# Performance work log

Measured on AMD Instinct MI355X. Metric: run time of the kernel, lower is better.

## Reference

```python
import jax, jax.numpy as jnp
import numpy as np
import math

N = 8192
NFEAT = 63
NHID = 1024
NLAYERS = 7
LAMBDA = 1.5
ALPHA = 0.7
NEG = -1e12


def setup_inputs() -> dict:
    key = jax.random.key(0)
    ks = jax.random.split(key, 12)
    x = jax.random.normal(ks[0], (N, NFEAT), dtype=jnp.float32)
    # dist acts as a (normalized) propagation matrix; scale by 1/N for numerical stability
    dist = jax.random.uniform(ks[1], (N, N), dtype=jnp.float32) / N
    adj = jax.random.randint(ks[2], (N, N), 0, 2, dtype=jnp.int32)
    # parameters
    fc_W = jax.random.normal(ks[3], (NFEAT, NHID), dtype=jnp.float32) * 0.1
    fc_b = jnp.zeros((NHID,), dtype=jnp.float32)
    stdv = 1.0 / math.sqrt(NHID)
    conv_W = jax.random.uniform(ks[4], (NLAYERS, NHID, NHID), dtype=jnp.float32,
                                minval=-stdv, maxval=stdv)
    gat_W = jax.random.normal(ks[5], (NHID, NHID), dtype=jnp.float32) * (1.414 / math.sqrt(NHID))
    gat_a = jax.random.normal(ks[6], (2 * NHID, 1), dtype=jnp.float32) * 0.05
    cls1_W = jax.random.normal(ks[7], (NHID, 64), dtype=jnp.float32) * (1.0 / math.sqrt(NHID))
    cls1_b = jnp.zeros((64,), dtype=jnp.float32)
    cls3_W = jax.random.normal(ks[8], (64, 1), dtype=jnp.float32) * 0.125
    cls3_b = jnp.zeros((1,), dtype=jnp.float32)
    return {"x": x, "dist": dist, "adj": adj, "fc_W": fc_W, "fc_b": fc_b,
            "conv_W": conv_W, "gat_W": gat_W, "gat_a": gat_a,
            "cls1_W": cls1_W, "cls1_b": cls1_b, "cls3_W": cls3_W, "cls3_b": cls3_b}


def _theta(l):
    return min(1.0, math.log(LAMBDA / l + 1.0))


def reference(x, dist, adj, fc_W, fc_b, conv_W, gat_W, gat_a, cls1_W, cls1_b, cls3_W, cls3_b):
    # eval mode: all dropouts are identity
    h = jax.nn.relu(x @ fc_W + fc_b)          # [N, H]
    h0 = h
    # GCNII-style propagation layers
    for i in range(NLAYERS):
        theta = _theta(i + 1)
        hi = dist @ h                          # [N, H] sparse-style propagation
        support = (1.0 - ALPHA) * hi + ALPHA * h0
        out = theta * (support @ conv_W[i]) + (1.0 - theta) * support + h
        h = jax.nn.relu(out)
    # GAT layer (l = 9). Faithful math, but computed without the N*N*2F tensor:
    # e_ij = leakyrelu(h_i' @ a1 + h_j' @ a2) with h' = h @ W
    hp = h @ gat_W                             # [N, H]
    a1 = gat_a[:NHID, 0]                       # [H]
    a2 = gat_a[NHID:, 0]                       # [H]
    e = jax.nn.leaky_relu(hp @ a1[:, None] + (hp @ a2[:, None]).T, negative_slope=0.2)  # [N, N]
    e = jnp.where(adj > 0, e, NEG)
    attention = jax.nn.softmax(e, axis=1)      # [N, N]
    theta = _theta(9)
    hi = attention @ h                         # note: attends over layer input h, not hp
    support = (1.0 - ALPHA) * hi + ALPHA * h0
    out = theta * (support @ gat_W) + (1.0 - theta) * support + h
    h = jax.nn.elu(out)
    h = jax.nn.relu(h @ cls1_W + cls1_b)
    out = jax.nn.sigmoid(h @ cls3_W + cls3_b)  # [N, 1]
    return out.squeeze(-1)                     # [N]
```

## Files before the change

### kernel.cpp

```cpp
#include <hip/hip_runtime.h>
#include <math.h>

#define NN 8192
#define NH 1024

typedef __bf16 bf16x8 __attribute__((ext_vector_type(8)));
typedef float floatx4 __attribute__((ext_vector_type(4)));
typedef unsigned short us8 __attribute__((ext_vector_type(8)));
typedef unsigned short us;

__device__ __forceinline__ unsigned short f2bf(float f) {
  unsigned int u = __float_as_uint(f);
  u += 0x7fffu + ((u >> 16) & 1u);
  return (unsigned short)(u >> 16);
}

__device__ __forceinline__ void async16(const void* g, void* l) {
  __builtin_amdgcn_global_load_lds(
      (__attribute__((address_space(1))) void*)(g),
      (__attribute__((address_space(3))) void*)(l), 16, 0, 0);
}

template<int EPI>
__global__ __launch_bounds__(256)
void gemm_db(const us* __restrict__ A, const us* __restrict__ Bt, int K,
             const float* __restrict__ aux, float* __restrict__ iof,
             us* __restrict__ outb, us* __restrict__ hTb, float theta)
{
  __shared__ __align__(16) us lsm[EPI == 1 ? 17408 : 16384];
  const int id = blockIdx.x;
  const int xcd = id & 7, slot = id >> 3;
  const int xt = slot & 7;
  const int yt = xcd + 8 * (slot >> 3);

  const int tid  = threadIdx.x;
  const int lane = tid & 63;
  const int wave = tid >> 6;
  const long tileM = (long)yt * 128;
  const long tileN = (long)xt * 128;
  const int wm = (wave & 1) * 64;
  const int wn = (wave >> 1) * 64;

  const us* gA0 = A + (tileM + (tid >> 2)) * (long)K + (tid & 3) * 8;
  const us* gA1 = gA0 + 64L * K;
  const us* gB0 = Bt + (tileN + (tid >> 2)) * (long)K + (tid & 3) * 8;
  const us* gB1 = gB0 + 64L * K;
  us* lA = lsm;
  us* lB = lsm + 8192;
  const int lo = tid * 8;

  const int fr = lane & 15;
  const int q8 = (lane >> 4) * 8;

  floatx4 zero4 = {0.f, 0.f, 0.f, 0.f};
  floatx4 acc[4][4];
#pragma unroll
  for (int i = 0; i < 4; ++i)
#pragma unroll
    for (int j = 0; j < 4; ++j) acc[i][j] = zero4;

  async16(gA0, lA + lo);
  async16(gA1, lA + lo + 2048);
  async16(gB0, lB + lo);
  async16(gB1, lB + lo + 2048);

  const int nkt = K >> 5;
  for (int kt = 0; kt < nkt; ++kt) {
    const int b = (kt & 1) << 12;
    __syncthreads();
    if (kt + 1 < nkt) {
      const int k0 = (kt + 1) << 5;
      const int b2 = b ^ 4096;
      async16(gA0 + k0, lA + b2 + lo);
      async16(gA1 + k0, lA + b2 + lo + 2048);
      async16(gB0 + k0, lB + b2 + lo);
      async16(gB1 + k0, lB + b2 + lo + 2048);
    }
    bf16x8 af[4], bfr[4];
#pragma unroll
    for (int i = 0; i < 4; ++i)
      af[i] = *(const bf16x8*)&lA[b + (wm + 16 * i + fr) * 32 + q8];
#pragma unroll
    for (int j = 0; j < 4; ++j)
      bfr[j] = *(const bf16x8*)&lB[b + (wn + 16 * j + fr) * 32 + q8];
#pragma unroll
    for (int i = 0; i < 4; ++i)
#pragma unroll
      for (int j = 0; j < 4; ++j)
        acc[i][j] = __builtin_amdgcn_mfma_f32_16x16x32_bf16(af[i], bfr[j], acc[i][j], 0, 0, 0);
  }

  if (EPI == 1) __syncthreads();
  us* ldsT = lsm;
  const int crow = (lane >> 4) * 4;
#pragma unroll
  for (int i = 0; i < 4; ++i) {
#pragma unroll
    for (int j = 0; j < 4; ++j) {
#pragma unroll
      for (int r = 0; r < 4; ++r) {
        int lr = wm + 16 * i + crow + r;
        int lc = wn + 16 * j + fr;
        long idx = (tileM + lr) * NH + tileN + lc;
        float v = acc[i][j][r];
        if (EPI == 0) {
          float s = 0.3f * v + 0.7f * aux[idx];
          iof[idx] = s;
          outb[idx] = f2bf(s);
        } else {
          float o = theta * v + (1.f - theta) * aux[idx] + iof[idx];
          o = (EPI == 1) ? fmaxf(o, 0.f) : (o > 0.f ? o : __expf(o) - 1.f);
          iof[idx] = o;
          if (EPI == 1) ldsT[lc * 136 + lr] = f2bf(o);
          if (EPI == 2) outb[idx] = f2bf(o);
        }
      }
    }
  }
  if (EPI == 1) {
    __syncthreads();
    int c = tid >> 1, half = tid & 1;
#pragma unroll
    for (int it = 0; it < 8; ++it) {
      int r = half * 64 + it * 8;
      us8 v = *(const us8*)&ldsT[c * 136 + r];
      *(us8*)&hTb[(tileN + c) * 8192L + tileM + r] = v;
    }
  }
}

__global__ __launch_bounds__(256)
void cls_gemm(const us* __restrict__ hb, const us* __restrict__ W1t,
              const float* __restrict__ b1, const float* __restrict__ W3,
              const float* __restrict__ b3, float* __restrict__ out)
{
  __shared__ __align__(16) us lA[4096];
  __shared__ __align__(16) us lB[2048];
  const int tid = threadIdx.x, lane = tid & 63, wave = tid >> 6;
  const long tileM = (long)blockIdx.x * 128;
  const us* gA0 = hb + (tileM + (tid >> 2)) * 1024L + (tid & 3) * 8;
  const us* gA1 = gA0 + 64 * 1024L;
  const us* gB0 = W1t + (tid >> 2) * 1024L + (tid & 3) * 8;
  const int fr = lane & 15, q8 = (lane >> 4) * 8;
  const int wm = wave * 32;

  floatx4 zero4 = {0.f, 0.f, 0.f, 0.f};
  floatx4 acc[2][4];
#pragma unroll
  for (int i = 0; i < 2; ++i)
#pragma unroll
    for (int j = 0; j < 4; ++j) acc[i][j] = zero4;

  for (int kt = 0; kt < 32; ++kt) {
    const int k0 = kt << 5;
    async16(gA0 + k0, lA + tid * 8);
    async16(gA1 + k0, lA + 2048 + tid * 8);
    async16(gB0 + k0, lB + tid * 8);
    __syncthreads();
    bf16x8 af[2], bfr[4];
#pragma unroll
    for (int i = 0; i < 2; ++i)
      af[i] = *(const bf16x8*)&lA[(wm + 16 * i + fr) * 32 + q8];
#pragma unroll
    for (int j = 0; j < 4; ++j)
      bfr[j] = *(const bf16x8*)&lB[(16 * j + fr) * 32 + q8];
#pragma unroll
    for (int i = 0; i < 2; ++i)
#pragma unroll
      for (int j = 0; j < 4; ++j)
        acc[i][j] = __builtin_amdgcn_mfma_f32_16x16x32_bf16(af[i], bfr[j], acc[i][j], 0, 0, 0);
    __syncthreads();
  }

  float b1v[4], w3v[4];
#pragma unroll
  for (int j = 0; j < 4; ++j) { b1v[j] = b1[16 * j + fr]; w3v[j] = W3[16 * j + fr]; }
  const float b3v = b3[0];
  const int crow = (lane >> 4) * 4;
#pragma unroll
  for (int i = 0; i < 2; ++i)
#pragma unroll
    for (int r = 0; r < 4; ++r) {
      float v = 0.f;
#pragma unroll
      for (int j = 0; j < 4; ++j)
        v += fmaxf(acc[i][j][r] + b1v[j], 0.f) * w3v[j];
      v += __shfl_xor(v, 1);
      v += __shfl_xor(v, 2);
      v += __shfl_xor(v, 4);
      v += __shfl_xor(v, 8);
      if (fr == 0)
        out[tileM + wm + 16 * i + crow + r] = 1.f / (1.f + __expf(-(v + b3v)));
    }
}

__global__ __launch_bounds__(256)
void transpose_f32_bf16(const float* __restrict__ src, us* __restrict__ dst,
                        int R, int C) {
  __shared__ float t[32][33];
  int tid = threadIdx.x;
  int tx = tid & 31, ty = tid >> 5;
  long r0 = (long)blockIdx.y * 32, c0 = (long)blockIdx.x * 32;
#pragma unroll
  for (int i = 0; i < 32; i += 8)
    t[ty + i][tx] = src[(r0 + ty + i) * C + c0 + tx];
  __syncthreads();
#pragma unroll
  for (int i = 0; i < 32; i += 8)
    dst[(c0 + ty + i) * R + r0 + tx] = f2bf(t[tx][ty + i]);
}

__global__ __launch_bounds__(256)
void f32_to_bf16_vec(const float* __restrict__ s, us* __restrict__ d) {
  long i = (blockIdx.x * 256L + threadIdx.x) * 4;
  float4 v = *(const float4*)(s + i);
  *(ushort4*)(d + i) = make_ushort4(f2bf(v.x), f2bf(v.y), f2bf(v.z), f2bf(v.w));
}

__global__ __launch_bounds__(256)
void fc_kernel(const float* __restrict__ x, const float* __restrict__ W,
               const float* __restrict__ b, float* __restrict__ h0f,
               float* __restrict__ hf) {
  __shared__ float xs[64];
  int row = blockIdx.x, tid = threadIdx.x;
  if (tid < 63) xs[tid] = x[row * 63 + tid];
  __syncthreads();
#pragma unroll
  for (int q = 0; q < 4; ++q) {
    int c = tid + q * 256;
    float s = b[c];
    for (int k = 0; k < 63; ++k) s += xs[k] * W[k * NH + c];
    s = fmaxf(s, 0.f);
    long idx = (long)row * NH + c;
    h0f[idx] = s;
    hf[idx] = s;
  }
}

__global__ __launch_bounds__(256)
void wv_kernel(const float* __restrict__ W, const float* __restrict__ a,
               float* __restrict__ va1, float* __restrict__ va2) {
  int k = blockIdx.x, tid = threadIdx.x;
  float s1 = 0.f, s2 = 0.f;
  for (int n = tid; n < NH; n += 256) {
    float w = W[(long)k * NH + n];
    s1 += w * a[n];
    s2 += w * a[NH + n];
  }
#pragma unroll
  for (int o = 32; o; o >>= 1) { s1 += __shfl_down(s1, o); s2 += __shfl_down(s2, o); }
  __shared__ float r1[4], r2[4];
  int wave = tid >> 6;
  if ((tid & 63) == 0) { r1[wave] = s1; r2[wave] = s2; }
  __syncthreads();
  if (tid == 0) {
    va1[k] = r1[0] + r1[1] + r1[2] + r1[3];
    va2[k] = r2[0] + r2[1] + r2[2] + r2[3];
  }
}

__global__ __launch_bounds__(256)
void fg_kernel(const float* __restrict__ h, const float* __restrict__ va1,
               const float* __restrict__ va2, float* __restrict__ fv,
               float* __restrict__ gv) {
  int row = blockIdx.x, tid = threadIdx.x;
  float s1 = 0.f, s2 = 0.f;
  for (int k = tid; k < NH; k += 256) {
    float v = h[(long)row * NH + k];
    s1 += v * va1[k];
    s2 += v * va2[k];
  }
#pragma unroll
  for (int o = 32; o; o >>= 1) { s1 += __shfl_down(s1, o); s2 += __shfl_down(s2, o); }
  __shared__ float r1[4], r2[4];
  int wave = tid >> 6;
  if ((tid & 63) == 0) { r1[wave] = s1; r2[wave] = s2; }
  __syncthreads();
  if (tid == 0) {
    fv[row] = r1[0] + r1[1] + r1[2] + r1[3];
    gv[row] = r2[0] + r2[1] + r2[2] + r2[3];
  }
}

__global__ __launch_bounds__(256)
void attn_ml(const int* __restrict__ adj, const float* __restrict__ f,
             const float* __restrict__ g, float* __restrict__ Mr,
             float* __restrict__ Lr) {
  const int row = blockIdx.x, tid = threadIdx.x;
  const float fi = f[row];
  const int4* arow = (const int4*)(adj + (long)row * NN);
  float m = -3.0e38f, s = 0.f;
  for (int c = tid; c < NN / 4; c += 256) {
    int4 a = arow[c];
    float4 gg = *(const float4*)(g + c * 4);
#pragma unroll
    for (int t = 0; t < 4; ++t) {
      int av = (t == 0) ? a.x : (t == 1) ? a.y : (t == 2) ? a.z : a.w;
      float gvv = (t == 0) ? gg.x : (t == 1) ? gg.y : (t == 2) ? gg.z : gg.w;
      if (av > 0) {
        float e = fi + gvv;
        e = e > 0.f ? e : 0.2f * e;
        if (e > m) { s = s * __expf(m - e) + 1.f; m = e; }
        else s += __expf(e - m);
      }
    }
  }
#pragma unroll
  for (int o = 32; o; o >>= 1) {
    float m2 = __shfl_down(m, o), s2 = __shfl_down(s, o);
    float mn = fmaxf(m, m2);
    s = s * __expf(m - mn) + s2 * __expf(m2 - mn);
    m = mn;
  }
  __shared__ float ms[4], ss[4];
  int wave = tid >> 6;
  if ((tid & 63) == 0) { ms[wave] = m; ss[wave] = s; }
  __syncthreads();
  if (tid == 0) {
    float mm = ms[0], sv = ss[0];
    for (int w = 1; w < 4; ++w) {
      float mn = fmaxf(mm, ms[w]);
      sv = sv * __expf(mm - mn) + ss[w] * __expf(ms[w] - mn);
      mm = mn;
    }
    Mr[row] = mm;
    Lr[row] = sv;
  }
}

__global__ __launch_bounds__(256)
void attn_p(const int* __restrict__ adj, const float* __restrict__ f,
            const float* __restrict__ g, const float* __restrict__ Mr,
            const float* __restrict__ Lr, us* __restrict__ P) {
  long gid = blockIdx.x * 256L + threadIdx.x;
  int row = (int)(gid >> 11);
  int jc = (int)(gid & 2047) * 4;
  float fi = f[row], m = Mr[row], l = Lr[row];
  bool uni = !(l > 0.f);
  float inv = uni ? 0.f : 1.f / l;
  int4 a = *(const int4*)(adj + ((long)row << 13) + jc);
  float4 gg = *(const float4*)(g + jc);
  float p[4];
#pragma unroll
  for (int t = 0; t < 4; ++t) {
    int av = (t == 0) ? a.x : (t == 1) ? a.y : (t == 2) ? a.z : a.w;
    float gvv = (t == 0) ? gg.x : (t == 1) ? gg.y : (t == 2) ? gg.z : gg.w;
    float e = fi + gvv;
    e = e > 0.f ? e : 0.2f * e;
    float pv = (av > 0) ? __expf(e - m) * inv : 0.f;
    if (uni) pv = 1.f / (float)NN;
    p[t] = pv;
  }
  *(ushort4*)(P + ((long)row << 13) + jc) =
      make_ushort4(f2bf(p[0]), f2bf(p[1]), f2bf(p[2]), f2bf(p[3]));
}

extern "C" void kernel_launch(void* const* d_in, const int* in_sizes, int n_in,
                              void* d_out, int out_size, void* d_ws, size_t ws_size,
                              hipStream_t stream) {
  const float* x      = (const float*)d_in[0];
  const float* dist   = (const float*)d_in[1];
  const int*   adj    = (const int*)d_in[2];
  const float* fc_W   = (const float*)d_in[3];
  const float* fc_b   = (const float*)d_in[4];
  const float* conv_W = (const float*)d_in[5];
  const float* gat_W  = (const float*)d_in[6];
  const float* gat_a  = (const float*)d_in[7];
  const float* cls1_W = (const float*)d_in[8];
  const float* cls1_b = (const float*)d_in[9];
  const float* cls3_W = (const float*)d_in[10];
  const float* cls3_b = (const float*)d_in[11];
  float* out = (float*)d_out;

  char* p = (char*)d_ws;
  auto alloc = [&](size_t bytes) {
    char* r = p;
    p += (bytes + 255) & ~(size_t)255;
    return r;
  };
  us* distb   = (us*)alloc((size_t)NN * NN * 2);
  float* h0f  = (float*)alloc((size_t)NN * NH * 4);
  float* hf   = (float*)alloc((size_t)NN * NH * 4);
  float* supf = (float*)alloc((size_t)NN * NH * 4);
  us* supb    = (us*)alloc((size_t)NN * NH * 2);
  us* hb      = (us*)alloc((size_t)NN * NH * 2);
  us* hTb     = (us*)alloc((size_t)NN * NH * 2);
  us* convWT  = (us*)alloc((size_t)7 * NH * NH * 2);
  us* gatWT   = (us*)alloc((size_t)NH * NH * 2);
  us* W1t     = (us*)alloc((size_t)64 * NH * 2);
  float* va1 = (float*)alloc(NH * 4);
  float* va2 = (float*)alloc(NH * 4);
  float* fv  = (float*)alloc(NN * 4);
  float* gv  = (float*)alloc(NN * 4);
  float* Mr  = (float*)alloc(NN * 4);
  float* Lr  = (float*)alloc(NN * 4);

  float th[7];
  for (int l = 0; l < 7; ++l) {
    float t = logf(1.5f / (float)(l + 1) + 1.f);
    th[l] = t < 1.f ? t : 1.f;
  }
  float th9 = logf(1.5f / 9.f + 1.f);

  f32_to_bf16_vec<<<(NN * (long)NN) / (4 * 256), 256, 0, stream>>>(dist, distb);
  for (int i = 0; i < 7; ++i)
    transpose_f32_bf16<<<dim3(32, 32), 256, 0, stream>>>(
        conv_W + (size_t)i * NH * NH, convWT + (size_t)i * NH * NH, NH, NH);
  transpose_f32_bf16<<<dim3(32, 32), 256, 0, stream>>>(gat_W, gatWT, NH, NH);
  transpose_f32_bf16<<<dim3(2, 32), 256, 0, stream>>>(cls1_W, W1t, NH, 64);

  fc_kernel<<<NN, 256, 0, stream>>>(x, fc_W, fc_b, h0f, hf);
  transpose_f32_bf16<<<dim3(NH / 32, NN / 32), 256, 0, stream>>>(hf, hTb, NN, NH);

  for (int l = 0; l < 7; ++l) {
    gemm_db<0><<<512, 256, 0, stream>>>(distb, hTb, NN, h0f, supf, supb, nullptr, 0.f);
    gemm_db<1><<<512, 256, 0, stream>>>(supb, convWT + (size_t)l * NH * NH, NH,
                                        supf, hf, nullptr, hTb, th[l]);
  }

  wv_kernel<<<NH, 256, 0, stream>>>(gat_W, gat_a, va1, va2);
  fg_kernel<<<NN, 256, 0, stream>>>(hf, va1, va2, fv, gv);
  attn_ml<<<NN, 256, 0, stream>>>(adj, fv, gv, Mr, Lr);
  attn_p<<<(NN * (long)NN) / (4 * 256), 256, 0, stream>>>(adj, fv, gv, Mr, Lr, distb);

  gemm_db<0><<<512, 256, 0, stream>>>(distb, hTb, NN, h0f, supf, supb, nullptr, 0.f);
  gemm_db<2><<<512, 256, 0, stream>>>(supb, gatWT, NH, supf, hf, hb, nullptr, th9);

  cls_gemm<<<64, 256, 0, stream>>>(hb, W1t, cls1_b, cls3_W, cls3_b, out);
}
```

Measured before the change: 2.510 ms.

## Add 256x128-tile GEMM with 4-stage async pipeline for propagation matmuls

```diff
diff --git a/kernel.cpp b/kernel.cpp
--- a/kernel.cpp
+++ b/kernel.cpp
@@ -19,6 +19,102 @@
   __builtin_amdgcn_global_load_lds(
       (__attribute__((address_space(1))) void*)(g),
       (__attribute__((address_space(3))) void*)(l), 16, 0, 0);
+}
+
+__global__ __launch_bounds__(256)
+void gemm_big(const us* __restrict__ A, const us* __restrict__ Bt,
+              const float* __restrict__ aux, float* __restrict__ supf,
+              us* __restrict__ supb)
+{
+  __shared__ __align__(16) us lsm[49152];
+  us* lB = lsm;
+  us* lA = lsm + 16384;
+
+  const int id = blockIdx.x;
+  const int yt = id & 31;
+  const int xt = id >> 5;
+
+  const int tid  = threadIdx.x;
+  const int lane = tid & 63;
+  const int wave = tid >> 6;
+  const long tileM = (long)yt * 256;
+  const long tileN = (long)xt * 128;
+  const int wm = (wave & 1) * 128;
+  const int wn = (wave >> 1) * 64;
+
+  const us* gAp = A + (tileM + (tid >> 2)) * 8192L + (tid & 3) * 8;
+  const us* gBp = Bt + (tileN + (tid >> 2)) * 8192L + (tid & 3) * 8;
+  const int lo = tid * 8;
+
+  const int fr = lane & 15;
+  const int q8 = (lane >> 4) * 8;
+
+  floatx4 zero4 = {0.f, 0.f, 0.f, 0.f};
+  floatx4 acc[8][4];
+#pragma unroll
+  for (int i = 0; i < 8; ++i)
+#pragma unroll
+    for (int j = 0; j < 4; ++j) acc[i][j] = zero4;
+
+#define STAGE_BIG(s, kf)                                                  \
+  {                                                                       \
+    const long ko = (long)(kf) << 5;                                      \
+    async16(gAp + ko, lA + (s)*8192 + lo);                                \
+    async16(gAp + 64 * 8192L + ko, lA + (s)*8192 + 2048 + lo);            \
+    async16(gAp + 128 * 8192L + ko, lA + (s)*8192 + 4096 + lo);           \
+    async16(gAp + 192 * 8192L + ko, lA + (s)*8192 + 6144 + lo);           \
+    async16(gBp + ko, lB + (s)*4096 + lo);                                \
+    async16(gBp + 64 * 8192L + ko, lB + (s)*4096 + 2048 + lo);            \
+  }
+
+#define COMP_BIG(s)                                                       \
+  {                                                                       \
+    bf16x8 af[8], bfr[4];                                                 \
+    _Pragma("unroll") for (int i = 0; i < 8; ++i)                         \
+        af[i] = *(const bf16x8*)&lA[(s)*8192 + (wm + 16 * i + fr) * 32 + q8]; \
+    _Pragma("unroll") for (int j = 0; j < 4; ++j)                         \
+        bfr[j] = *(const bf16x8*)&lB[(s)*4096 + (wn + 16 * j + fr) * 32 + q8]; \
+    _Pragma("unroll") for (int i = 0; i < 8; ++i)                         \
+        _Pragma("unroll") for (int j = 0; j < 4; ++j)                     \
+            acc[i][j] = __builtin_amdgcn_mfma_f32_16x16x32_bf16(          \
+                af[i], bfr[j], acc[i][j], 0, 0, 0);                       \
+  }
+
+#define WAITB asm volatile("s_waitcnt vmcnt(12)\n\ts_barrier" ::: "memory")
+
+  STAGE_BIG(0, 0)
+  STAGE_BIG(1, 1)
+  STAGE_BIG(2, 2)
+
+  for (int kt = 0; kt < 256; kt += 4) {
+    int k3 = kt + 3; if (k3 > 255) k3 = 255;
+    int k4 = kt + 4; if (k4 > 255) k4 = 255;
+    int k5 = kt + 5; if (k5 > 255) k5 = 255;
+    int k6 = kt + 6; if (k6 > 255) k6 = 255;
+    WAITB; STAGE_BIG(3, k3) COMP_BIG(0)
+    WAITB; STAGE_BIG(0, k4) COMP_BIG(1)
+    WAITB; STAGE_BIG(1, k5) COMP_BIG(2)
+    WAITB; STAGE_BIG(2, k6) COMP_BIG(3)
+  }
+  asm volatile("s_waitcnt vmcnt(0)" ::: "memory");
+
+  const int crow = (lane >> 4) * 4;
+#pragma unroll
+  for (int i = 0; i < 8; ++i)
+#pragma unroll
+    for (int j = 0; j < 4; ++j)
+#pragma unroll
+      for (int r = 0; r < 4; ++r) {
+        long row = tileM + wm + 16 * i + crow + r;
+        long col = tileN + wn + 16 * j + fr;
+        long idx = row * NH + col;
+        float s = 0.3f * acc[i][j][r] + 0.7f * aux[idx];
+        supf[idx] = s;
+        supb[idx] = f2bf(s);
+      }
+#undef STAGE_BIG
+#undef COMP_BIG
+#undef WAITB
 }
 
 template<int EPI>
@@ -90,7 +186,7 @@
         acc[i][j] = __builtin_amdgcn_mfma_f32_16x16x32_bf16(af[i], bfr[j], acc[i][j], 0, 0, 0);
   }
 
-  if (EPI == 1) __syncthreads();
+  __syncthreads();
   us* ldsT = lsm;
   const int crow = (lane >> 4) * 4;
 #pragma unroll
@@ -102,18 +198,11 @@
         int lr = wm + 16 * i + crow + r;
         int lc = wn + 16 * j + fr;
         long idx = (tileM + lr) * NH + tileN + lc;
-        float v = acc[i][j][r];
-        if (EPI == 0) {
-          float s = 0.3f * v + 0.7f * aux[idx];
-          iof[idx] = s;
-          outb[idx] = f2bf(s);
-        } else {
-          float o = theta * v + (1.f - theta) * aux[idx] + iof[idx];
-          o = (EPI == 1) ? fmaxf(o, 0.f) : (o > 0.f ? o : __expf(o) - 1.f);
-          iof[idx] = o;
-          if (EPI == 1) ldsT[lc * 136 + lr] = f2bf(o);
-          if (EPI == 2) outb[idx] = f2bf(o);
-        }
+        float o = theta * acc[i][j][r] + (1.f - theta) * aux[idx] + iof[idx];
+        o = (EPI == 1) ? fmaxf(o, 0.f) : (o > 0.f ? o : __expf(o) - 1.f);
+        iof[idx] = o;
+        if (EPI == 1) ldsT[lc * 136 + lr] = f2bf(o);
+        if (EPI == 2) outb[idx] = f2bf(o);
       }
     }
   }
@@ -413,7 +502,7 @@
   transpose_f32_bf16<<<dim3(NH / 32, NN / 32), 256, 0, stream>>>(hf, hTb, NN, NH);
 
   for (int l = 0; l < 7; ++l) {
-    gemm_db<0><<<512, 256, 0, stream>>>(distb, hTb, NN, h0f, supf, supb, nullptr, 0.f);
+    gemm_big<<<256, 256, 0, stream>>>(distb, hTb, h0f, supf, supb);
     gemm_db<1><<<512, 256, 0, stream>>>(supb, convWT + (size_t)l * NH * NH, NH,
                                         supf, hf, nullptr, hTb, th[l]);
   }
@@ -423,7 +512,7 @@
   attn_ml<<<NN, 256, 0, stream>>>(adj, fv, gv, Mr, Lr);
   attn_p<<<(NN * (long)NN) / (4 * 256), 256, 0, stream>>>(adj, fv, gv, Mr, Lr, distb);
 
-  gemm_db<0><<<512, 256, 0, stream>>>(distb, hTb, NN, h0f, supf, supb, nullptr, 0.f);
+  gemm_big<<<256, 256, 0, stream>>>(distb, hTb, h0f, supf, supb);
   gemm_db<2><<<512, 256, 0, stream>>>(supb, gatWT, NH, supf, hf, hb, nullptr, th9);
 
   cls_gemm<<<64, 256, 0, stream>>>(hb, W1t, cls1_b, cls3_W, cls3_b, out);
```

New measurement: 2.425 ms. 1.03x faster.
